# Kernel tuning notes

Hardware: AMD Instinct MI355X
Metric: run time of the kernel (lower is better)

The kernel has to match this reference:

```python
import jax, jax.numpy as jnp
import numpy as np

D_MODEL = 256
N_HEADS = 8
D_HEAD = D_MODEL // N_HEADS
SCALE = D_HEAD ** -0.5
LN_EPS = 1e-5


def _layernorm(x, gamma, beta):
    mu = jnp.mean(x, axis=-1, keepdims=True)
    var = jnp.mean(jnp.square(x - mu), axis=-1, keepdims=True)
    return (x - mu) * jax.lax.rsqrt(var + LN_EPS) * gamma + beta


def setup_inputs() -> dict:
    key = jax.random.key(0)
    ks = jax.random.split(key, 8)
    B, N_q, N_kv = 2, 1024, 8192
    q = jax.random.normal(ks[0], (B, N_q, D_MODEL), dtype=jnp.float32)
    kv = jax.random.normal(ks[1], (B, N_kv, D_MODEL), dtype=jnp.float32)
    attn_bias = jax.random.normal(ks[2], (B, N_HEADS, N_q, N_kv), dtype=jnp.float32)
    s = D_MODEL ** -0.5
    Wq = jax.random.normal(ks[3], (D_MODEL, D_MODEL), dtype=jnp.float32) * s
    Wk = jax.random.normal(ks[4], (D_MODEL, D_MODEL), dtype=jnp.float32) * s
    Wv = jax.random.normal(ks[5], (D_MODEL, D_MODEL), dtype=jnp.float32) * s
    Wo = jax.random.normal(ks[6], (D_MODEL, D_MODEL), dtype=jnp.float32) * s
    gamma_q = jnp.ones((D_MODEL,), jnp.float32)
    beta_q = jnp.zeros((D_MODEL,), jnp.float32)
    gamma_kv = jnp.ones((D_MODEL,), jnp.float32)
    beta_kv = jnp.zeros((D_MODEL,), jnp.float32)
    return dict(q=q, kv=kv, attn_bias=attn_bias, Wq=Wq, Wk=Wk, Wv=Wv, Wo=Wo,
                gamma_q=gamma_q, beta_q=beta_q, gamma_kv=gamma_kv, beta_kv=beta_kv)


def reference(q, kv, attn_bias, Wq, Wk, Wv, Wo, gamma_q, beta_q, gamma_kv, beta_kv):
    B, N_q, D = q.shape
    N_kv = kv.shape[1]
    q_n = _layernorm(q, gamma_q, beta_q)
    kv_n = _layernorm(kv, gamma_kv, beta_kv)
    # nn.Linear(x) = x @ W.T ; reshape to (B, H, N, dh)
    Q = (q_n @ Wq.T).reshape(B, N_q, N_HEADS, D_HEAD).transpose(0, 2, 1, 3)
    K = (kv_n @ Wk.T).reshape(B, N_kv, N_HEADS, D_HEAD).transpose(0, 2, 1, 3)
    V = (kv_n @ Wv.T).reshape(B, N_kv, N_HEADS, D_HEAD).transpose(0, 2, 1, 3)
    scores = jnp.einsum('bhqd,bhkd->bhqk', Q, K) * SCALE + attn_bias
    attn = jax.nn.softmax(scores, axis=-1)
    out = jnp.einsum('bhqk,bhkd->bhqd', attn, V)
    out = out.transpose(0, 2, 1, 3).reshape(B, N_q, D)
    return q + out @ Wo.T
```

## Files before the change

### kernel.cpp

```cpp
#include <hip/hip_runtime.h>
#include <hip/hip_bf16.h>
#include <stdint.h>

#define H 8
#define NQ 1024
#define NKV 8192
#define DM 256
#define DH 32
#define KVBLK 128
#define KSPLIT 8
#define QBLK 128
#define NITER (NKV / KSPLIT / KVBLK)
#define SCALE 0.17677669529663687f

typedef __attribute__((ext_vector_type(8))) __bf16 bf16x8;
typedef __attribute__((ext_vector_type(4))) float f32x4;

__device__ inline unsigned short f2bf(float f) {
  unsigned int u = __builtin_bit_cast(unsigned int, f);
  u = (u + 0x7FFFu + ((u >> 16) & 1u)) >> 16;
  return (unsigned short)u;
}

__global__ void prep_kernel(const float* __restrict__ q, const float* __restrict__ kv,
                            const float* __restrict__ gq, const float* __restrict__ bq,
                            const float* __restrict__ gkv, const float* __restrict__ bkv,
                            const float* __restrict__ Wq, const float* __restrict__ Wk,
                            const float* __restrict__ Wv, const float* __restrict__ Wo,
                            unsigned short* __restrict__ qn, unsigned short* __restrict__ kvn,
                            unsigned short* __restrict__ Wqb, unsigned short* __restrict__ Wkb,
                            unsigned short* __restrict__ Wvb, unsigned short* __restrict__ Wob) {
  int bx = blockIdx.x;
  if (bx < 256) {
    int widx = bx >> 6, blk = bx & 63;
    const float* src; unsigned short* dst;
    if (widx == 0)      { src = Wq; dst = Wqb; }
    else if (widx == 1) { src = Wk; dst = Wkb; }
    else if (widx == 2) { src = Wv; dst = Wvb; }
    else                { src = Wo; dst = Wob; }
    int i = (blk * 256 + threadIdx.x) * 4;
    float4 v = *(const float4*)(src + i);
    unsigned int lo = (unsigned int)f2bf(v.x) | ((unsigned int)f2bf(v.y) << 16);
    unsigned int hi = (unsigned int)f2bf(v.z) | ((unsigned int)f2bf(v.w) << 16);
    *(uint2*)(dst + i) = make_uint2(lo, hi);
    return;
  }
  int row = (bx - 256) * 64 + (threadIdx.x >> 2);
  int l4 = threadIdx.x & 3;
  const float* src; const float* ga; const float* be; unsigned short* dst;
  if (row < 2048) {
    src = q + (long)row * DM; ga = gq; be = bq; dst = qn + (long)row * DM;
  } else {
    int r2 = row - 2048;
    src = kv + (long)r2 * DM; ga = gkv; be = bkv; dst = kvn + (long)r2 * DM;
  }
  int c0 = l4 * 64;
  float s = 0.f, ss = 0.f;
  float4 xv[16];
#pragma unroll
  for (int i = 0; i < 16; i++) {
    float4 v = *(const float4*)(src + c0 + i * 4);
    xv[i] = v;
    s += v.x + v.y + v.z + v.w;
    ss += v.x * v.x + v.y * v.y + v.z * v.z + v.w * v.w;
  }
  s += __shfl_xor(s, 1, 4);  s += __shfl_xor(s, 2, 4);
  ss += __shfl_xor(ss, 1, 4); ss += __shfl_xor(ss, 2, 4);
  float mean = s * (1.0f / 256.0f);
  float var = ss * (1.0f / 256.0f) - mean * mean;
  float rs = 1.0f / sqrtf(var + 1e-5f);
#pragma unroll
  for (int i = 0; i < 8; i++) {
    float4 a = xv[2 * i], b = xv[2 * i + 1];
    float4 g0 = *(const float4*)(ga + c0 + i * 8);
    float4 g1 = *(const float4*)(ga + c0 + i * 8 + 4);
    float4 b0 = *(const float4*)(be + c0 + i * 8);
    float4 b1 = *(const float4*)(be + c0 + i * 8 + 4);
    unsigned short t[8];
    t[0] = f2bf((a.x - mean) * rs * g0.x + b0.x);
    t[1] = f2bf((a.y - mean) * rs * g0.y + b0.y);
    t[2] = f2bf((a.z - mean) * rs * g0.z + b0.z);
    t[3] = f2bf((a.w - mean) * rs * g0.w + b0.w);
    t[4] = f2bf((b.x - mean) * rs * g1.x + b1.x);
    t[5] = f2bf((b.y - mean) * rs * g1.y + b1.y);
    t[6] = f2bf((b.z - mean) * rs * g1.z + b1.z);
    t[7] = f2bf((b.w - mean) * rs * g1.w + b1.w);
    unsigned int u0 = (unsigned int)t[0] | ((unsigned int)t[1] << 16);
    unsigned int u1 = (unsigned int)t[2] | ((unsigned int)t[3] << 16);
    unsigned int u2 = (unsigned int)t[4] | ((unsigned int)t[5] << 16);
    unsigned int u3 = (unsigned int)t[6] | ((unsigned int)t[7] << 16);
    *(uint4*)(dst + c0 + i * 8) = make_uint4(u0, u1, u2, u3);
  }
}

__global__ void proj_all_kernel(const unsigned short* __restrict__ qn, const unsigned short* __restrict__ kvn,
                                const unsigned short* __restrict__ Wqb, const unsigned short* __restrict__ Wkb,
                                const unsigned short* __restrict__ Wvb,
                                unsigned short* __restrict__ Qw, unsigned short* __restrict__ Kw,
                                unsigned short* __restrict__ Vtw) {
  int bx = blockIdx.x;
  const unsigned short* X; const unsigned short* Wb; unsigned short* out;
  int Nper, mode, mb;
  if (bx < 32)       { X = qn;  Wb = Wqb; out = Qw;  Nper = NQ;  mode = 0; mb = bx; }
  else if (bx < 288) { X = kvn; Wb = Wkb; out = Kw;  Nper = NKV; mode = 0; mb = bx - 32; }
  else               { X = kvn; Wb = Wvb; out = Vtw; Nper = NKV; mode = 1; mb = bx - 288; }

  int w = threadIdx.x >> 6, lane = threadIdx.x & 63;
  int c = lane & 15, g = lane >> 4;
  int mbase = mb * 64 + w * 16;
  f32x4 acc[16];
#pragma unroll
  for (int i = 0; i < 16; i++) acc[i] = (f32x4){0.f, 0.f, 0.f, 0.f};
  const unsigned short* arow = X + (long)(mbase + c) * DM + g * 8;
#pragma unroll
  for (int ks = 0; ks < 8; ks++) {
    bf16x8 af = *(const bf16x8*)(arow + ks * 32);
#pragma unroll
    for (int nt = 0; nt < 16; nt++) {
      bf16x8 bf = *(const bf16x8*)(Wb + (long)(nt * 16 + c) * DM + ks * 32 + g * 8);
      acc[nt] = __builtin_amdgcn_mfma_f32_16x16x32_bf16(af, bf, acc[nt], 0, 0, 0);
    }
  }
#pragma unroll
  for (int nt = 0; nt < 16; nt++) {
#pragma unroll
    for (int r = 0; r < 4; r++) {
      int m = mbase + 4 * g + r;
      int n = nt * 16 + c;
      int b = (m >= Nper) ? 1 : 0;
      int i = m - b * Nper;
      int h = n >> 5, dd = n & 31;
      long idx;
      if (mode == 0) idx = ((long)(b * H + h) * Nper + i) * DH + dd;
      else           idx = ((long)(b * H + h) * DH + dd) * (long)Nper + i;
      out[idx] = f2bf(acc[nt][r]);
    }
  }
}

__global__ __launch_bounds__(512, 4) void attn_kernel(
    const unsigned short* __restrict__ Qw, const unsigned short* __restrict__ Kw,
    const unsigned short* __restrict__ Vtw, const float* __restrict__ bias,
    float* __restrict__ Opart, float* __restrict__ Mpart, float* __restrict__ Lpart) {
  __shared__ __align__(16) unsigned short Klds[KVBLK * 40];
  __shared__ __align__(16) unsigned short Vlds[DH * 136];
  __shared__ __align__(16) unsigned short Plds[8][16 * 136];

  int bx = blockIdx.x;
  int s = bx & 7, qt = (bx >> 3) & 7, bh = bx >> 6;
  int tid = threadIdx.x;
  int w = tid >> 6, lane = tid & 63, c = lane & 15, g = lane >> 4;

  const f32x4 fzero = {0.f, 0.f, 0.f, 0.f};

  bf16x8 qfrag = *(const bf16x8*)(Qw + ((long)(bh * NQ + qt * QBLK + w * 16 + c)) * DH + g * 8);

  const float* brow = bias + ((long)bh * NQ + qt * QBLK + w * 16 + c) * (long)NKV + 4 * g;

  const unsigned short* Kbase = Kw + ((long)bh * NKV) * DH;
  const unsigned short* Vbase = Vtw + ((long)bh * DH) * NKV;

  float m_run = -1e30f;
  float l_run = 0.f;
  f32x4 oacc[2] = {fzero, fzero};

#pragma unroll 1
  for (int it = 0; it < NITER; it++) {
    int k0 = (it * KSPLIT + s) * KVBLK;

    f32x4 bfrag[8];
#pragma unroll
    for (int t = 0; t < 8; t++)
      bfrag[t] = *(const f32x4*)(brow + k0 + t * 16);

    {
      int krow = tid >> 2, kq4 = tid & 3;
      *(uint4*)(&Klds[krow * 40 + kq4 * 8]) =
          *(const uint4*)(Kbase + (long)(k0 + krow) * DH + kq4 * 8);
      int vd = tid >> 4, vq16 = tid & 15;
      *(uint4*)(&Vlds[vd * 136 + vq16 * 8]) =
          *(const uint4*)(Vbase + (long)vd * NKV + k0 + vq16 * 8);
    }
    __syncthreads();

    f32x4 sacc[8];
#pragma unroll
    for (int t = 0; t < 8; t++) {
      bf16x8 kf = *(const bf16x8*)(&Klds[(t * 16 + c) * 40 + g * 8]);
      sacc[t] = __builtin_amdgcn_mfma_f32_16x16x32_bf16(kf, qfrag, fzero, 0, 0, 0);
    }
#pragma unroll
    for (int t = 0; t < 8; t++) {
#pragma unroll
      for (int r = 0; r < 4; r++)
        sacc[t][r] = fmaf(sacc[t][r], SCALE, bfrag[t][r]);
    }

    float v = -1e30f;
#pragma unroll
    for (int t = 0; t < 8; t++)
      v = fmaxf(v, fmaxf(fmaxf(sacc[t][0], sacc[t][1]), fmaxf(sacc[t][2], sacc[t][3])));
    v = fmaxf(v, __shfl_xor(v, 16));
    v = fmaxf(v, __shfl_xor(v, 32));
    float mnew = fmaxf(m_run, v);
    float al = __expf(m_run - mnew);
    m_run = mnew;
    float rsum = 0.f;
#pragma unroll
    for (int t = 0; t < 8; t++) {
      float p0 = __expf(sacc[t][0] - mnew);
      float p1 = __expf(sacc[t][1] - mnew);
      float p2 = __expf(sacc[t][2] - mnew);
      float p3 = __expf(sacc[t][3] - mnew);
      rsum += (p0 + p1) + (p2 + p3);
      uint2 pk;
      pk.x = (unsigned int)f2bf(p0) | ((unsigned int)f2bf(p1) << 16);
      pk.y = (unsigned int)f2bf(p2) | ((unsigned int)f2bf(p3) << 16);
      *(uint2*)(&Plds[w][c * 136 + t * 16 + 4 * g]) = pk;
    }
    rsum += __shfl_xor(rsum, 16);
    rsum += __shfl_xor(rsum, 32);
    l_run = l_run * al + rsum;

    float alq[4];
#pragma unroll
    for (int r = 0; r < 4; r++) alq[r] = __shfl(al, 4 * g + r);
#pragma unroll
    for (int r = 0; r < 4; r++) { oacc[0][r] *= alq[r]; oacc[1][r] *= alq[r]; }

#pragma unroll
    for (int ch = 0; ch < 4; ch++) {
      bf16x8 pf = *(const bf16x8*)(&Plds[w][c * 136 + ch * 32 + g * 8]);
#pragma unroll
      for (int dt = 0; dt < 2; dt++) {
        bf16x8 vf = *(const bf16x8*)(&Vlds[(dt * 16 + c) * 136 + ch * 32 + g * 8]);
        oacc[dt] = __builtin_amdgcn_mfma_f32_16x16x32_bf16(pf, vf, oacc[dt], 0, 0, 0);
      }
    }
    __syncthreads();
  }
  float* Op = Opart + (long)bx * (QBLK * 32);
#pragma unroll
  for (int dt = 0; dt < 2; dt++)
#pragma unroll
    for (int r = 0; r < 4; r++)
      Op[(w * 16 + 4 * g + r) * 32 + dt * 16 + c] = oacc[dt][r];
  if (g == 0) {
    Mpart[(long)bx * QBLK + w * 16 + c] = m_run;
    Lpart[(long)bx * QBLK + w * 16 + c] = l_run;
  }
}

__global__ void merge_outproj_kernel(const float* __restrict__ Opart, const float* __restrict__ Mpart,
                                     const float* __restrict__ Lpart, const unsigned short* __restrict__ Wob,
                                     const float* __restrict__ qin, float* __restrict__ out) {
  __shared__ __align__(16) unsigned short OmT[16][264];

  int bx = blockIdx.x;
  int b = bx >> 6, t6 = bx & 63;
  int qt8 = t6 >> 3;
  int rbase = (t6 & 7) * 16;
  int tid = threadIdx.x;

  int row16 = tid >> 4;
  int d0 = (tid & 15) * 2;
  int rowin = rbase + row16;
#pragma unroll 1
  for (int h = 0; h < 8; h++) {
    long pbase = (((long)(b * 8 + h) * 8 + qt8)) * 8;
    float mg = -1e30f, ms[8];
#pragma unroll
    for (int si = 0; si < 8; si++) {
      ms[si] = Mpart[(pbase + si) * QBLK + rowin];
      mg = fmaxf(mg, ms[si]);
    }
    float Lg = 0.f;
    float o0 = 0.f, o1 = 0.f;
#pragma unroll
    for (int si = 0; si < 8; si++) {
      float wsc = __expf(ms[si] - mg);
      Lg += Lpart[(pbase + si) * QBLK + rowin] * wsc;
      const float* op = Opart + (pbase + si) * (QBLK * 32) + rowin * 32 + d0;
      o0 += op[0] * wsc;
      o1 += op[1] * wsc;
    }
    float inv = 1.0f / Lg;
    unsigned int u = (unsigned int)f2bf(o0 * inv) | ((unsigned int)f2bf(o1 * inv) << 16);
    *(unsigned int*)(&OmT[row16][h * 32 + d0]) = u;
  }
  __syncthreads();

  int w = tid >> 6, lane = tid & 63;
  int c = lane & 15, g = lane >> 4;
  long mglob = (long)b * NQ + t6 * 16;
  f32x4 acc[4];
#pragma unroll
  for (int i = 0; i < 4; i++) acc[i] = (f32x4){0.f, 0.f, 0.f, 0.f};
#pragma unroll
  for (int ks = 0; ks < 8; ks++) {
    bf16x8 af = *(const bf16x8*)(&OmT[c][ks * 32 + g * 8]);
#pragma unroll
    for (int j = 0; j < 4; j++) {
      int nt = w * 4 + j;
      bf16x8 bf = *(const bf16x8*)(Wob + (long)(nt * 16 + c) * DM + ks * 32 + g * 8);
      acc[j] = __builtin_amdgcn_mfma_f32_16x16x32_bf16(af, bf, acc[j], 0, 0, 0);
    }
  }
#pragma unroll
  for (int j = 0; j < 4; j++) {
#pragma unroll
    for (int r = 0; r < 4; r++) {
      long m = mglob + 4 * g + r;
      int n = (w * 4 + j) * 16 + c;
      out[m * DM + n] = qin[m * DM + n] + acc[j][r];
    }
  }
}

extern "C" void kernel_launch(void* const* d_in, const int* in_sizes, int n_in,
                              void* d_out, int out_size, void* d_ws, size_t ws_size,
                              hipStream_t stream) {
  (void)in_sizes; (void)n_in; (void)out_size; (void)ws_size;
  const float* q    = (const float*)d_in[0];
  const float* kv   = (const float*)d_in[1];
  const float* bias = (const float*)d_in[2];
  const float* Wq   = (const float*)d_in[3];
  const float* Wk   = (const float*)d_in[4];
  const float* Wv   = (const float*)d_in[5];
  const float* Wo   = (const float*)d_in[6];
  const float* gq   = (const float*)d_in[7];
  const float* bq   = (const float*)d_in[8];
  const float* gkv  = (const float*)d_in[9];
  const float* bkv  = (const float*)d_in[10];
  float* out = (float*)d_out;

  char* ws = (char*)d_ws;
  size_t off = 0;
  auto alloc = [&](size_t bytes) -> void* {
    void* p = ws + off;
    off += (bytes + 255) & ~(size_t)255;
    return p;
  };
  unsigned short* Wqb  = (unsigned short*)alloc(65536 * 2);
  unsigned short* Wkb  = (unsigned short*)alloc(65536 * 2);
  unsigned short* Wvb  = (unsigned short*)alloc(65536 * 2);
  unsigned short* Wob  = (unsigned short*)alloc(65536 * 2);
  unsigned short* qn   = (unsigned short*)alloc((size_t)2048 * 256 * 2);
  unsigned short* kvn  = (unsigned short*)alloc((size_t)16384 * 256 * 2);
  unsigned short* Qw   = (unsigned short*)alloc((size_t)2048 * 256 * 2);
  unsigned short* Kw   = (unsigned short*)alloc((size_t)16384 * 256 * 2);
  unsigned short* Vtw  = (unsigned short*)alloc((size_t)16384 * 256 * 2);
  float* Opart = (float*)alloc((size_t)1024 * 128 * 32 * 4);
  float* Mpart = (float*)alloc((size_t)1024 * 128 * 4);
  float* Lpart = (float*)alloc((size_t)1024 * 128 * 4);

  prep_kernel<<<544, 256, 0, stream>>>(q, kv, gq, bq, gkv, bkv, Wq, Wk, Wv, Wo,
                                       qn, kvn, Wqb, Wkb, Wvb, Wob);

  proj_all_kernel<<<544, 256, 0, stream>>>(qn, kvn, Wqb, Wkb, Wvb, Qw, Kw, Vtw);

  attn_kernel<<<1024, 512, 0, stream>>>(Qw, Kw, Vtw, bias, Opart, Mpart, Lpart);

  merge_outproj_kernel<<<128, 256, 0, stream>>>(Opart, Mpart, Lpart, Wob, q, out);
}
```

Measured before the change: 218.5 us.

## Fuse all stages into one cooperative persistent kernel with grid syncs

```diff
diff --git a/kernel.cpp b/kernel.cpp
--- a/kernel.cpp
+++ b/kernel.cpp
@@ -1,6 +1,9 @@
 #include <hip/hip_runtime.h>
 #include <hip/hip_bf16.h>
+#include <hip/hip_cooperative_groups.h>
 #include <stdint.h>
+
+namespace cg = cooperative_groups;
 
 #define H 8
 #define NQ 1024
@@ -22,37 +25,40 @@
   return (unsigned short)u;
 }
 
-__global__ void prep_kernel(const float* __restrict__ q, const float* __restrict__ kv,
-                            const float* __restrict__ gq, const float* __restrict__ bq,
-                            const float* __restrict__ gkv, const float* __restrict__ bkv,
-                            const float* __restrict__ Wq, const float* __restrict__ Wk,
-                            const float* __restrict__ Wv, const float* __restrict__ Wo,
-                            unsigned short* __restrict__ qn, unsigned short* __restrict__ kvn,
-                            unsigned short* __restrict__ Wqb, unsigned short* __restrict__ Wkb,
-                            unsigned short* __restrict__ Wvb, unsigned short* __restrict__ Wob) {
-  int bx = blockIdx.x;
-  if (bx < 256) {
-    int widx = bx >> 6, blk = bx & 63;
+struct Params {
+  const float *q, *kv, *bias, *Wq, *Wk, *Wv, *Wo, *gq, *bq, *gkv, *bkv;
+  unsigned short *qn, *kvn, *Wqb, *Wkb, *Wvb, *Wob, *Qw, *Kw, *Vtw;
+  float *Opart, *Mpart, *Lpart, *out;
+};
+
+__device__ inline void phase0(int bx, int tid, const Params& p) {
+  if (bx < 32) {
+    long i = ((long)bx * 512 + tid) * 16;
+    int widx = (int)(i >> 16);
+    int off = (int)(i & 65535);
     const float* src; unsigned short* dst;
-    if (widx == 0)      { src = Wq; dst = Wqb; }
-    else if (widx == 1) { src = Wk; dst = Wkb; }
-    else if (widx == 2) { src = Wv; dst = Wvb; }
-    else                { src = Wo; dst = Wob; }
-    int i = (blk * 256 + threadIdx.x) * 4;
-    float4 v = *(const float4*)(src + i);
-    unsigned int lo = (unsigned int)f2bf(v.x) | ((unsigned int)f2bf(v.y) << 16);
-    unsigned int hi = (unsigned int)f2bf(v.z) | ((unsigned int)f2bf(v.w) << 16);
-    *(uint2*)(dst + i) = make_uint2(lo, hi);
+    if (widx == 0)      { src = p.Wq; dst = p.Wqb; }
+    else if (widx == 1) { src = p.Wk; dst = p.Wkb; }
+    else if (widx == 2) { src = p.Wv; dst = p.Wvb; }
+    else                { src = p.Wo; dst = p.Wob; }
+#pragma unroll
+    for (int j = 0; j < 4; j++) {
+      float4 v = *(const float4*)(src + off + j * 4);
+      unsigned int lo = (unsigned int)f2bf(v.x) | ((unsigned int)f2bf(v.y) << 16);
+      unsigned int hi = (unsigned int)f2bf(v.z) | ((unsigned int)f2bf(v.w) << 16);
+      *(uint2*)(dst + off + j * 4) = make_uint2(lo, hi);
+    }
     return;
   }
-  int row = (bx - 256) * 64 + (threadIdx.x >> 2);
-  int l4 = threadIdx.x & 3;
+  if (bx >= 176) return;
+  int row = (bx - 32) * 128 + (tid >> 2);
+  int l4 = tid & 3;
   const float* src; const float* ga; const float* be; unsigned short* dst;
   if (row < 2048) {
-    src = q + (long)row * DM; ga = gq; be = bq; dst = qn + (long)row * DM;
+    src = p.q + (long)row * DM; ga = p.gq; be = p.bq; dst = p.qn + (long)row * DM;
   } else {
     int r2 = row - 2048;
-    src = kv + (long)r2 * DM; ga = gkv; be = bkv; dst = kvn + (long)r2 * DM;
+    src = p.kv + (long)r2 * DM; ga = p.gkv; be = p.bkv; dst = p.kvn + (long)r2 * DM;
   }
   int c0 = l4 * 64;
   float s = 0.f, ss = 0.f;
@@ -93,19 +99,14 @@
   }
 }
 
-__global__ void proj_all_kernel(const unsigned short* __restrict__ qn, const unsigned short* __restrict__ kvn,
-                                const unsigned short* __restrict__ Wqb, const unsigned short* __restrict__ Wkb,
-                                const unsigned short* __restrict__ Wvb,
-                                unsigned short* __restrict__ Qw, unsigned short* __restrict__ Kw,
-                                unsigned short* __restrict__ Vtw) {
-  int bx = blockIdx.x;
+__device__ inline void proj_unit(int unit, int t, const Params& p) {
   const unsigned short* X; const unsigned short* Wb; unsigned short* out;
   int Nper, mode, mb;
-  if (bx < 32)       { X = qn;  Wb = Wqb; out = Qw;  Nper = NQ;  mode = 0; mb = bx; }
-  else if (bx < 288) { X = kvn; Wb = Wkb; out = Kw;  Nper = NKV; mode = 0; mb = bx - 32; }
-  else               { X = kvn; Wb = Wvb; out = Vtw; Nper = NKV; mode = 1; mb = bx - 288; }
-
-  int w = threadIdx.x >> 6, lane = threadIdx.x & 63;
+  if (unit < 32)       { X = p.qn;  Wb = p.Wqb; out = p.Qw;  Nper = NQ;  mode = 0; mb = unit; }
+  else if (unit < 288) { X = p.kvn; Wb = p.Wkb; out = p.Kw;  Nper = NKV; mode = 0; mb = unit - 32; }
+  else                 { X = p.kvn; Wb = p.Wvb; out = p.Vtw; Nper = NKV; mode = 1; mb = unit - 288; }
+
+  int w = t >> 6, lane = t & 63;
   int c = lane & 15, g = lane >> 4;
   int mbase = mb * 64 + w * 16;
   f32x4 acc[16];
@@ -138,27 +139,22 @@
   }
 }
 
-__global__ __launch_bounds__(512, 4) void attn_kernel(
-    const unsigned short* __restrict__ Qw, const unsigned short* __restrict__ Kw,
-    const unsigned short* __restrict__ Vtw, const float* __restrict__ bias,
-    float* __restrict__ Opart, float* __restrict__ Mpart, float* __restrict__ Lpart) {
+__device__ inline void attn_unit(int u, int tid, const Params& p) {
   __shared__ __align__(16) unsigned short Klds[KVBLK * 40];
   __shared__ __align__(16) unsigned short Vlds[DH * 136];
   __shared__ __align__(16) unsigned short Plds[8][16 * 136];
 
-  int bx = blockIdx.x;
-  int s = bx & 7, qt = (bx >> 3) & 7, bh = bx >> 6;
-  int tid = threadIdx.x;
+  int s = u & 7, qt = (u >> 3) & 7, bh = u >> 6;
   int w = tid >> 6, lane = tid & 63, c = lane & 15, g = lane >> 4;
 
   const f32x4 fzero = {0.f, 0.f, 0.f, 0.f};
 
-  bf16x8 qfrag = *(const bf16x8*)(Qw + ((long)(bh * NQ + qt * QBLK + w * 16 + c)) * DH + g * 8);
-
-  const float* brow = bias + ((long)bh * NQ + qt * QBLK + w * 16 + c) * (long)NKV + 4 * g;
-
-  const unsigned short* Kbase = Kw + ((long)bh * NKV) * DH;
-  const unsigned short* Vbase = Vtw + ((long)bh * DH) * NKV;
+  bf16x8 qfrag = *(const bf16x8*)(p.Qw + ((long)(bh * NQ + qt * QBLK + w * 16 + c)) * DH + g * 8);
+
+  const float* brow = p.bias + ((long)bh * NQ + qt * QBLK + w * 16 + c) * (long)NKV + 4 * g;
+
+  const unsigned short* Kbase = p.Kw + ((long)bh * NKV) * DH;
+  const unsigned short* Vbase = p.Vtw + ((long)bh * DH) * NKV;
 
   float m_run = -1e30f;
   float l_run = 0.f;
@@ -239,31 +235,27 @@
     }
     __syncthreads();
   }
-  float* Op = Opart + (long)bx * (QBLK * 32);
+  float* Op = p.Opart + (long)u * (QBLK * 32);
 #pragma unroll
   for (int dt = 0; dt < 2; dt++)
 #pragma unroll
     for (int r = 0; r < 4; r++)
       Op[(w * 16 + 4 * g + r) * 32 + dt * 16 + c] = oacc[dt][r];
   if (g == 0) {
-    Mpart[(long)bx * QBLK + w * 16 + c] = m_run;
-    Lpart[(long)bx * QBLK + w * 16 + c] = l_run;
-  }
-}
-
-__global__ void merge_outproj_kernel(const float* __restrict__ Opart, const float* __restrict__ Mpart,
-                                     const float* __restrict__ Lpart, const unsigned short* __restrict__ Wob,
-                                     const float* __restrict__ qin, float* __restrict__ out) {
+    p.Mpart[(long)u * QBLK + w * 16 + c] = m_run;
+    p.Lpart[(long)u * QBLK + w * 16 + c] = l_run;
+  }
+}
+
+__device__ inline void merge_unit(int bx, int tid, const Params& p) {
   __shared__ __align__(16) unsigned short OmT[16][264];
 
-  int bx = blockIdx.x;
   int b = bx >> 6, t6 = bx & 63;
   int qt8 = t6 >> 3;
   int rbase = (t6 & 7) * 16;
-  int tid = threadIdx.x;
-
-  int row16 = tid >> 4;
-  int d0 = (tid & 15) * 2;
+
+  int row16 = tid >> 5;
+  int dcol = tid & 31;
   int rowin = rbase + row16;
 #pragma unroll 1
   for (int h = 0; h < 8; h++) {
@@ -271,95 +263,128 @@
     float mg = -1e30f, ms[8];
 #pragma unroll
     for (int si = 0; si < 8; si++) {
-      ms[si] = Mpart[(pbase + si) * QBLK + rowin];
+      ms[si] = p.Mpart[(pbase + si) * QBLK + rowin];
       mg = fmaxf(mg, ms[si]);
     }
-    float Lg = 0.f;
-    float o0 = 0.f, o1 = 0.f;
+    float Lg = 0.f, o = 0.f;
 #pragma unroll
     for (int si = 0; si < 8; si++) {
       float wsc = __expf(ms[si] - mg);
-      Lg += Lpart[(pbase + si) * QBLK + rowin] * wsc;
-      const float* op = Opart + (pbase + si) * (QBLK * 32) + rowin * 32 + d0;
-      o0 += op[0] * wsc;
-      o1 += op[1] * wsc;
-    }
-    float inv = 1.0f / Lg;
-    unsigned int u = (unsigned int)f2bf(o0 * inv) | ((unsigned int)f2bf(o1 * inv) << 16);
-    *(unsigned int*)(&OmT[row16][h * 32 + d0]) = u;
+      Lg += p.Lpart[(pbase + si) * QBLK + rowin] * wsc;
+      o += p.Opart[(pbase + si) * (QBLK * 32) + rowin * 32 + dcol] * wsc;
+    }
+    OmT[row16][h * 32 + dcol] = f2bf(o / Lg);
   }
   __syncthreads();
 
   int w = tid >> 6, lane = tid & 63;
   int c = lane & 15, g = lane >> 4;
   long mglob = (long)b * NQ + t6 * 16;
-  f32x4 acc[4];
-#pragma unroll
-  for (int i = 0; i < 4; i++) acc[i] = (f32x4){0.f, 0.f, 0.f, 0.f};
+  f32x4 acc[2];
+  acc[0] = (f32x4){0.f, 0.f, 0.f, 0.f};
+  acc[1] = (f32x4){0.f, 0.f, 0.f, 0.f};
 #pragma unroll
   for (int ks = 0; ks < 8; ks++) {
     bf16x8 af = *(const bf16x8*)(&OmT[c][ks * 32 + g * 8]);
 #pragma unroll
-    for (int j = 0; j < 4; j++) {
-      int nt = w * 4 + j;
-      bf16x8 bf = *(const bf16x8*)(Wob + (long)(nt * 16 + c) * DM + ks * 32 + g * 8);
+    for (int j = 0; j < 2; j++) {
+      int nt = w * 2 + j;
+      bf16x8 bf = *(const bf16x8*)(p.Wob + (long)(nt * 16 + c) * DM + ks * 32 + g * 8);
       acc[j] = __builtin_amdgcn_mfma_f32_16x16x32_bf16(af, bf, acc[j], 0, 0, 0);
     }
   }
 #pragma unroll
-  for (int j = 0; j < 4; j++) {
+  for (int j = 0; j < 2; j++) {
 #pragma unroll
     for (int r = 0; r < 4; r++) {
       long m = mglob + 4 * g + r;
-      int n = (w * 4 + j) * 16 + c;
-      out[m * DM + n] = qin[m * DM + n] + acc[j][r];
-    }
-  }
+      int n = (w * 2 + j) * 16 + c;
+      p.out[m * DM + n] = p.q[m * DM + n] + acc[j][r];
+    }
+  }
+}
+
+__global__ __launch_bounds__(512, 4) void fused_kernel(Params p) {
+  cg::grid_group grid = cg::this_grid();
+  int bx = blockIdx.x, tid = threadIdx.x;
+
+  phase0(bx, tid, p);
+  grid.sync();
+
+  if (bx < 272) proj_unit(bx * 2 + (tid >> 8), tid & 255, p);
+  grid.sync();
+
+  attn_unit(bx, tid, p);
+  __syncthreads();
+  attn_unit(bx + 512, tid, p);
+  grid.sync();
+
+  if (bx < 128) merge_unit(bx, tid, p);
+}
+
+__global__ __launch_bounds__(512, 4) void prep512_kernel(Params p) {
+  phase0(blockIdx.x, threadIdx.x, p);
+}
+__global__ __launch_bounds__(512, 4) void proj512_kernel(Params p) {
+  proj_unit(blockIdx.x * 2 + (threadIdx.x >> 8), threadIdx.x & 255, p);
+}
+__global__ __launch_bounds__(512, 4) void attn512_kernel(Params p) {
+  attn_unit(blockIdx.x, threadIdx.x, p);
+}
+__global__ __launch_bounds__(512, 4) void merge512_kernel(Params p) {
+  merge_unit(blockIdx.x, threadIdx.x, p);
 }
 
 extern "C" void kernel_launch(void* const* d_in, const int* in_sizes, int n_in,
                               void* d_out, int out_size, void* d_ws, size_t ws_size,
                               hipStream_t stream) {
   (void)in_sizes; (void)n_in; (void)out_size; (void)ws_size;
-  const float* q    = (const float*)d_in[0];
-  const float* kv   = (const float*)d_in[1];
-  const float* bias = (const float*)d_in[2];
-  const float* Wq   = (const float*)d_in[3];
-  const float* Wk   = (const float*)d_in[4];
-  const float* Wv   = (const float*)d_in[5];
-  const float* Wo   = (const float*)d_in[6];
-  const float* gq   = (const float*)d_in[7];
-  const float* bq   = (const float*)d_in[8];
-  const float* gkv  = (const float*)d_in[9];
-  const float* bkv  = (const float*)d_in[10];
-  float* out = (float*)d_out;
 
   char* ws = (char*)d_ws;
   size_t off = 0;
   auto alloc = [&](size_t bytes) -> void* {
-    void* p = ws + off;
+    void* ptr = ws + off;
     off += (bytes + 255) & ~(size_t)255;
-    return p;
+    return ptr;
   };
-  unsigned short* Wqb  = (unsigned short*)alloc(65536 * 2);
-  unsigned short* Wkb  = (unsigned short*)alloc(65536 * 2);
-  unsigned short* Wvb  = (unsigned short*)alloc(65536 * 2);
-  unsigned short* Wob  = (unsigned short*)alloc(65536 * 2);
-  unsigned short* qn   = (unsigned short*)alloc((size_t)2048 * 256 * 2);
-  unsigned short* kvn  = (unsigned short*)alloc((size_t)16384 * 256 * 2);
-  unsigned short* Qw   = (unsigned short*)alloc((size_t)2048 * 256 * 2);
-  unsigned short* Kw   = (unsigned short*)alloc((size_t)16384 * 256 * 2);
-  unsigned short* Vtw  = (unsigned short*)alloc((size_t)16384 * 256 * 2);
-  float* Opart = (float*)alloc((size_t)1024 * 128 * 32 * 4);
-  float* Mpart = (float*)alloc((size_t)1024 * 128 * 4);
-  float* Lpart = (float*)alloc((size_t)1024 * 128 * 4);
-
-  prep_kernel<<<544, 256, 0, stream>>>(q, kv, gq, bq, gkv, bkv, Wq, Wk, Wv, Wo,
-                                       qn, kvn, Wqb, Wkb, Wvb, Wob);
-
-  proj_all_kernel<<<544, 256, 0, stream>>>(qn, kvn, Wqb, Wkb, Wvb, Qw, Kw, Vtw);
-
-  attn_kernel<<<1024, 512, 0, stream>>>(Qw, Kw, Vtw, bias, Opart, Mpart, Lpart);
-
-  merge_outproj_kernel<<<128, 256, 0, stream>>>(Opart, Mpart, Lpart, Wob, q, out);
-}
+
+  Params p;
+  p.q    = (const float*)d_in[0];
+  p.kv   = (const float*)d_in[1];
+  p.bias = (const float*)d_in[2];
+  p.Wq   = (const float*)d_in[3];
+  p.Wk   = (const float*)d_in[4];
+  p.Wv   = (const float*)d_in[5];
+  p.Wo   = (const float*)d_in[6];
+  p.gq   = (const float*)d_in[7];
+  p.bq   = (const float*)d_in[8];
+  p.gkv  = (const float*)d_in[9];
+  p.bkv  = (const float*)d_in[10];
+  p.out  = (float*)d_out;
+
+  p.Wqb  = (unsigned short*)alloc(65536 * 2);
+  p.Wkb  = (unsigned short*)alloc(65536 * 2);
+  p.Wvb  = (unsigned short*)alloc(65536 * 2);
+  p.Wob  = (unsigned short*)alloc(65536 * 2);
+  p.qn   = (unsigned short*)alloc((size_t)2048 * 256 * 2);
+  p.kvn  = (unsigned short*)alloc((size_t)16384 * 256 * 2);
+  p.Qw   = (unsigned short*)alloc((size_t)2048 * 256 * 2);
+  p.Kw   = (unsigned short*)alloc((size_t)16384 * 256 * 2);
+  p.Vtw  = (unsigned short*)alloc((size_t)16384 * 256 * 2);
+  p.Opart = (float*)alloc((size_t)1024 * 128 * 32 * 4);
+  p.Mpart = (float*)alloc((size_t)1024 * 128 * 4);
+  p.Lpart = (float*)alloc((size_t)1024 * 128 * 4);
+
+  void* kargs[] = { &p };
+  hipError_t err = hipLaunchCooperativeKernel(
+      reinterpret_cast<const void*>(fused_kernel),
+      dim3(512), dim3(512), kargs, 0, stream);
+
+  if (err != hipSuccess) {
+    (void)hipGetLastError();
+    prep512_kernel<<<176, 512, 0, stream>>>(p);
+    proj512_kernel<<<272, 512, 0, stream>>>(p);
+    attn512_kernel<<<1024, 512, 0, stream>>>(p);
+    merge512_kernel<<<128, 512, 0, stream>>>(p);
+  }
+}
```

Result: slower. 426.3 us (+95.1%).
